# Kernel tuning notes

Measured on AMD Instinct MI355X. Metric: run time of the kernel, lower is better.

Reference implementation:

```python
import jax, jax.numpy as jnp
import numpy as np


def setup_inputs() -> dict:
    key = jax.random.key(0)
    k1, k2 = jax.random.split(key)
    B, C, T = 16, 256, 512
    x = jax.random.normal(k1, (B, C, T), dtype=jnp.float32)
    duration = jax.random.randint(k2, (B, T), 0, 8).astype(jnp.int64)
    return {"x": x, "duration": duration}


def reference(x, duration):
    """LengthRegulator: repeat each phoneme vector duration[b, t] times,
    pad ragged results to the max mel length, zero-fill padding.
    x: [B, C, T] float, duration: [B, T] int. Returns ([B, C, L], mel_len[B]).
    """
    B, C, T = x.shape
    dur = jnp.maximum(duration, 0)                      # torch max(expand_size, 0)
    cum = jnp.cumsum(dur, axis=1)                       # [B, T] exclusive->inclusive cumsum
    mel_len = cum[:, -1]                                # [B]
    max_len = int(jnp.max(mel_len))                     # pad(output) pads to batch max
    frames = jnp.arange(max_len)                        # [L]
    # frame j of batch b comes from phoneme index = searchsorted(cum[b], j, 'right')
    idx = jax.vmap(lambda c: jnp.searchsorted(c, frames, side='right'))(cum)  # [B, L]
    idx = jnp.clip(idx, 0, T - 1)
    xt = jnp.transpose(x, (0, 2, 1))                    # [B, T, C]
    out = jnp.take_along_axis(xt, idx[:, :, None], axis=1)  # [B, L, C]
    mask = frames[None, :] < mel_len[:, None]           # [B, L]
    out = jnp.where(mask[:, :, None], out, jnp.zeros((), dtype=out.dtype))
    out = jnp.transpose(out, (0, 2, 1))                 # [B, C, L]
    return out, mel_len
```

## Files before the change

kernel.cpp:

```cpp
#include <hip/hip_runtime.h>

#define BB 16
#define CC 256
#define TT 512

__global__ __launch_bounds__(TT) void lr_scan_kernel(
    const int* __restrict__ dur,
    int* __restrict__ ws_mel,
    int* __restrict__ ws_idx,
    float* __restrict__ out_mel,
    int L)
{
    __shared__ int s[TT];
    const int b = blockIdx.x;
    const int t = threadIdx.x;

    int d = dur[b * TT + t];
    if (d < 0) d = 0;
    s[t] = d;
    __syncthreads();

    #pragma unroll
    for (int off = 1; off < TT; off <<= 1) {
        int v = (t >= off) ? s[t - off] : 0;
        __syncthreads();
        s[t] += v;
        __syncthreads();
    }

    const int cum = s[t];
    const int start = cum - d;

    int* idx = ws_idx + (size_t)b * L;
    for (int f = start; f < cum; ++f) idx[f] = t;

    if (t == TT - 1) {
        ws_mel[b] = cum;
        out_mel[b] = (float)cum;
    }
}

__global__ __launch_bounds__(256) void lr_gather_kernel(
    const float* __restrict__ x,
    const int* __restrict__ ws_mel,
    const int* __restrict__ ws_idx,
    float* __restrict__ out,
    int L)
{
    const int f = blockIdx.x * 256 + threadIdx.x;
    const int c = blockIdx.y;
    const int b = blockIdx.z;
    if (f >= L) return;

    const int ml = ws_mel[b];
    float v = 0.0f;
    if (f < ml) {
        const int idx = ws_idx[(size_t)b * L + f];
        v = x[((size_t)b * CC + c) * TT + idx];
    }
    out[((size_t)b * CC + c) * (size_t)L + f] = v;
}

extern "C" void kernel_launch(void* const* d_in, const int* in_sizes, int n_in,
                              void* d_out, int out_size, void* d_ws, size_t ws_size,
                              hipStream_t stream)
{
    const float* x  = (const float*)d_in[0];
    const int* dur  = (const int*)d_in[1];
    float* out      = (float*)d_out;

    const int L = (out_size - BB) / (BB * CC);

    int* ws_mel = (int*)d_ws;
    int* ws_idx = ws_mel + BB;
    float* out_mel = out + (size_t)BB * CC * L;

    lr_scan_kernel<<<BB, TT, 0, stream>>>(dur, ws_mel, ws_idx, out_mel, L);

    dim3 grid((L + 255) / 256, CC, BB);
    lr_gather_kernel<<<grid, 256, 0, stream>>>(x, ws_mel, ws_idx, out, L);
}
```

Before: 82.63 us.

## Use wave-shuffle scan and vectorized multi-channel gather with index reuse

Replaces the shared-memory Hillis-Steele scan with a wavefront shuffle scan plus a per-wave offset sum, which cuts barrier count. The gather kernel now has each thread handle four frames across a chunk of 16 channels. It loads the indices once as an int4 and reuses them for every channel, then writes float4 stores. This reduces index reloads and the number of store instructions, but the grid is smaller, which may lower occupancy.

```diff
diff --git a/kernel.cpp b/kernel.cpp
--- a/kernel.cpp
+++ b/kernel.cpp
@@ -3,6 +3,9 @@
 #define BB 16
 #define CC 256
 #define TT 512
+#define CSPLIT 16
+#define CCHUNK (CC / CSPLIT)
+#define FTILE 1024
 
 __global__ __launch_bounds__(TT) void lr_scan_kernel(
     const int* __restrict__ dur,
@@ -11,24 +14,29 @@
     float* __restrict__ out_mel,
     int L)
 {
-    __shared__ int s[TT];
+    __shared__ int wsum[TT / 64];
     const int b = blockIdx.x;
     const int t = threadIdx.x;
 
     int d = dur[b * TT + t];
     if (d < 0) d = 0;
-    s[t] = d;
+
+    int v = d;
+    #pragma unroll
+    for (int off = 1; off < 64; off <<= 1) {
+        int o = __shfl_up(v, off, 64);
+        if ((t & 63) >= off) v += o;
+    }
+    const int wid = t >> 6;
+    if ((t & 63) == 63) wsum[wid] = v;
     __syncthreads();
 
+    int woff = 0;
     #pragma unroll
-    for (int off = 1; off < TT; off <<= 1) {
-        int v = (t >= off) ? s[t - off] : 0;
-        __syncthreads();
-        s[t] += v;
-        __syncthreads();
-    }
+    for (int w = 0; w < TT / 64; ++w)
+        if (w < wid) woff += wsum[w];
 
-    const int cum = s[t];
+    const int cum = v + woff;
     const int start = cum - d;
 
     int* idx = ws_idx + (size_t)b * L;
@@ -47,18 +55,42 @@
     float* __restrict__ out,
     int L)
 {
-    const int f = blockIdx.x * 256 + threadIdx.x;
-    const int c = blockIdx.y;
-    const int b = blockIdx.z;
-    if (f >= L) return;
+    const int b  = blockIdx.z;
+    const int c0 = blockIdx.y * CCHUNK;
+    const int f0 = blockIdx.x * FTILE + threadIdx.x * 4;
+    if (f0 >= L) return;
 
     const int ml = ws_mel[b];
-    float v = 0.0f;
-    if (f < ml) {
-        const int idx = ws_idx[(size_t)b * L + f];
-        v = x[((size_t)b * CC + c) * TT + idx];
+    const int* __restrict__ idxp = ws_idx + (size_t)b * L;
+    const float* __restrict__ xb = x + ((size_t)b * CC + c0) * TT;
+    float* __restrict__ ob = out + ((size_t)b * CC + c0) * (size_t)L;
+
+    if (((L & 3) == 0) && (f0 + 3 < L)) {
+        const int4 id4 = *(const int4*)(idxp + f0);
+        const bool m0 = (f0 + 0) < ml;
+        const bool m1 = (f0 + 1) < ml;
+        const bool m2 = (f0 + 2) < ml;
+        const bool m3 = (f0 + 3) < ml;
+        #pragma unroll
+        for (int cc = 0; cc < CCHUNK; ++cc) {
+            const float* __restrict__ xr = xb + (size_t)cc * TT;
+            float4 v;
+            v.x = m0 ? xr[id4.x] : 0.0f;
+            v.y = m1 ? xr[id4.y] : 0.0f;
+            v.z = m2 ? xr[id4.z] : 0.0f;
+            v.w = m3 ? xr[id4.w] : 0.0f;
+            *(float4*)(ob + (size_t)cc * L + f0) = v;
+        }
+    } else {
+        const int fend = (f0 + 4 < L) ? (f0 + 4) : L;
+        for (int cc = 0; cc < CCHUNK; ++cc) {
+            for (int f = f0; f < fend; ++f) {
+                float v = 0.0f;
+                if (f < ml) v = xb[(size_t)cc * TT + idxp[f]];
+                ob[(size_t)cc * L + f] = v;
+            }
+        }
     }
-    out[((size_t)b * CC + c) * (size_t)L + f] = v;
 }
 
 extern "C" void kernel_launch(void* const* d_in, const int* in_sizes, int n_in,
@@ -77,6 +109,6 @@
 
     lr_scan_kernel<<<BB, TT, 0, stream>>>(dur, ws_mel, ws_idx, out_mel, L);
 
-    dim3 grid((L + 255) / 256, CC, BB);
+    dim3 grid((L + FTILE - 1) / FTILE, CSPLIT, BB);
     lr_gather_kernel<<<grid, 256, 0, stream>>>(x, ws_mel, ws_idx, out, L);
 }
```

New measurement: 90.79 us. +9.9%, slower.

## Fuse duration scan and gather into one kernel with LDS-staged rows

Applied to the files above, without the earlier changes.

Replaces the separate scan and gather kernels with one fused kernel. Each block recomputes the duration prefix sum with wavefront shuffles, stages four channel rows of x in LDS, builds the frame-to-phoneme index map for its frame tile in LDS, and writes float4-vectorized outputs. This removes the second launch, the global index workspace round-trip and the scattered global gathers. In exchange every block redoes the scan, and the launch now covers only 64 channel groups per batch.

```diff
diff --git a/kernel.cpp b/kernel.cpp
--- a/kernel.cpp
+++ b/kernel.cpp
@@ -3,80 +3,115 @@
 #define BB 16
 #define CC 256
 #define TT 512
+#define CCH 4
+#define FT 1024
+#define NTH 256
 
-__global__ __launch_bounds__(TT) void lr_scan_kernel(
+__global__ __launch_bounds__(NTH) void lr_fused_kernel(
+    const float* __restrict__ x,
     const int* __restrict__ dur,
-    int* __restrict__ ws_mel,
-    int* __restrict__ ws_idx,
-    float* __restrict__ out_mel,
-    int L)
-{
-    __shared__ int s[TT];
-    const int b = blockIdx.x;
-    const int t = threadIdx.x;
-
-    int d = dur[b * TT + t];
-    if (d < 0) d = 0;
-    s[t] = d;
-    __syncthreads();
-
-    #pragma unroll
-    for (int off = 1; off < TT; off <<= 1) {
-        int v = (t >= off) ? s[t - off] : 0;
-        __syncthreads();
-        s[t] += v;
-        __syncthreads();
-    }
-
-    const int cum = s[t];
-    const int start = cum - d;
-
-    int* idx = ws_idx + (size_t)b * L;
-    for (int f = start; f < cum; ++f) idx[f] = t;
-
-    if (t == TT - 1) {
-        ws_mel[b] = cum;
-        out_mel[b] = (float)cum;
-    }
-}
-
-__global__ __launch_bounds__(256) void lr_gather_kernel(
-    const float* __restrict__ x,
-    const int* __restrict__ ws_mel,
-    const int* __restrict__ ws_idx,
     float* __restrict__ out,
     int L)
 {
-    const int f = blockIdx.x * 256 + threadIdx.x;
-    const int c = blockIdx.y;
-    const int b = blockIdx.z;
-    if (f >= L) return;
+    __shared__ int   lds_idx[FT];
+    __shared__ float lds_x[CCH * TT];
+    __shared__ int   wsum[NTH / 64];
 
-    const int ml = ws_mel[b];
-    float v = 0.0f;
-    if (f < ml) {
-        const int idx = ws_idx[(size_t)b * L + f];
-        v = x[((size_t)b * CC + c) * TT + idx];
+    const int tid   = threadIdx.x;
+    const int b     = blockIdx.z;
+    const int c0    = blockIdx.y * CCH;
+    const int fbase = blockIdx.x * FT;
+
+    *(int4*)(lds_idx + tid * 4) = make_int4(0, 0, 0, 0);
+
+    int2 dp = *(const int2*)(dur + b * TT + tid * 2);
+    const int d0 = dp.x < 0 ? 0 : dp.x;
+    const int d1 = dp.y < 0 ? 0 : dp.y;
+    int v = d0 + d1;
+    #pragma unroll
+    for (int off = 1; off < 64; off <<= 1) {
+        int o = __shfl_up(v, off, 64);
+        if ((tid & 63) >= off) v += o;
     }
-    out[((size_t)b * CC + c) * (size_t)L + f] = v;
+    const int wid = tid >> 6;
+    if ((tid & 63) == 63) wsum[wid] = v;
+
+    const float* __restrict__ xb = x + ((size_t)b * CC + c0) * TT;
+    const float4 xv0 = *(const float4*)(xb + tid * 4);
+    const float4 xv1 = *(const float4*)(xb + 1024 + tid * 4);
+    *(float4*)(lds_x + tid * 4) = xv0;
+    *(float4*)(lds_x + 1024 + tid * 4) = xv1;
+
+    __syncthreads();
+
+    int woff = 0, ml = 0;
+    #pragma unroll
+    for (int w = 0; w < NTH / 64; ++w) {
+        const int s = wsum[w];
+        if (w < wid) woff += s;
+        ml += s;
+    }
+    const int cum1   = woff + v;
+    const int cum0   = cum1 - d1;
+    const int start0 = cum0 - d0;
+
+    const int fend = fbase + FT;
+    {
+        int lo = start0 > fbase ? start0 : fbase;
+        int hi = cum0 < fend ? cum0 : fend;
+        for (int f = lo; f < hi; ++f) lds_idx[f - fbase] = tid * 2;
+        lo = cum0 > fbase ? cum0 : fbase;
+        hi = cum1 < fend ? cum1 : fend;
+        for (int f = lo; f < hi; ++f) lds_idx[f - fbase] = tid * 2 + 1;
+    }
+    __syncthreads();
+
+    const int f0 = fbase + tid * 4;
+    if (f0 < L) {
+        const int4 id4 = *(const int4*)(lds_idx + tid * 4);
+        const bool m0 = (f0 + 0) < ml;
+        const bool m1 = (f0 + 1) < ml;
+        const bool m2 = (f0 + 2) < ml;
+        const bool m3 = (f0 + 3) < ml;
+        float* __restrict__ ob = out + ((size_t)b * CC + c0) * (size_t)L + f0;
+        if (((L & 3) == 0) && (f0 + 3 < L)) {
+            #pragma unroll
+            for (int cc = 0; cc < CCH; ++cc) {
+                const float* __restrict__ xr = lds_x + cc * TT;
+                float4 o;
+                o.x = m0 ? xr[id4.x] : 0.0f;
+                o.y = m1 ? xr[id4.y] : 0.0f;
+                o.z = m2 ? xr[id4.z] : 0.0f;
+                o.w = m3 ? xr[id4.w] : 0.0f;
+                *(float4*)(ob + (size_t)cc * L) = o;
+            }
+        } else {
+            const int nf = (L - f0) < 4 ? (L - f0) : 4;
+            for (int cc = 0; cc < CCH; ++cc) {
+                const float* __restrict__ xr = lds_x + cc * TT;
+                for (int j = 0; j < nf; ++j) {
+                    const int f = f0 + j;
+                    const int id = lds_idx[tid * 4 + j];
+                    ob[(size_t)cc * L + j] = (f < ml) ? xr[id] : 0.0f;
+                }
+            }
+        }
+    }
+
+    if (fbase == 0 && blockIdx.y == 0 && tid == 0)
+        out[(size_t)BB * CC * L + b] = (float)ml;
 }
 
 extern "C" void kernel_launch(void* const* d_in, const int* in_sizes, int n_in,
                               void* d_out, int out_size, void* d_ws, size_t ws_size,
                               hipStream_t stream)
 {
-    const float* x  = (const float*)d_in[0];
-    const int* dur  = (const int*)d_in[1];
-    float* out      = (float*)d_out;
+    const float* x = (const float*)d_in[0];
+    const int* dur = (const int*)d_in[1];
+    float* out     = (float*)d_out;
 
     const int L = (out_size - BB) / (BB * CC);
 
-    int* ws_mel = (int*)d_ws;
-    int* ws_idx = ws_mel + BB;
-    float* out_mel = out + (size_t)BB * CC * L;
-
-    lr_scan_kernel<<<BB, TT, 0, stream>>>(dur, ws_mel, ws_idx, out_mel, L);
-
-    dim3 grid((L + 255) / 256, CC, BB);
-    lr_gather_kernel<<<grid, 256, 0, stream>>>(x, ws_mel, ws_idx, out, L);
+    dim3 grid((L + FT - 1) / FT, CC / CCH, BB);
+    lr_fused_kernel<<<grid, NTH, 0, stream>>>(x, dur, out, L);
 }
```

Result: faster. 77.26 us (-6.5%).
